# Optimization experiments

Hardware: AMD Instinct MI355X
Metric: run time of the kernel (lower is better)

Reference implementation:

```python
import jax, jax.numpy as jnp
import numpy as np
import math

N_PATCH = 32768
DIM = 512
L_TOK = 64
W_SIZE = 64
STRIDE = 32


def setup_inputs() -> dict:
    key = jax.random.key(0)
    ks = jax.random.split(key, 12)
    d = DIM
    inp = {
        'feats': jax.random.normal(ks[0], (N_PATCH, d), dtype=jnp.float32),
        'coords': jax.random.uniform(ks[1], (N_PATCH, 2), dtype=jnp.float32),
        'mask': jnp.zeros((N_PATCH,), dtype=bool),
        'z': jax.random.normal(ks[2], (L_TOK, d), dtype=jnp.float32),
        'Wq': jax.random.normal(ks[3], (d, d), dtype=jnp.float32) / math.sqrt(d),
        'Wk': jax.random.normal(ks[4], (d, d), dtype=jnp.float32) / math.sqrt(d),
        'Wv': jax.random.normal(ks[5], (d, d), dtype=jnp.float32) / math.sqrt(d),
        'w1': jax.random.normal(ks[6], (d, 2), dtype=jnp.float32) / math.sqrt(2.0),
        'b1': jnp.zeros((d,), dtype=jnp.float32),
        'w2': jax.random.normal(ks[7], (d, d), dtype=jnp.float32) / math.sqrt(d),
        'b2': jnp.zeros((d,), dtype=jnp.float32),
        'Wo': jax.random.normal(ks[8], (d, d), dtype=jnp.float32) / math.sqrt(d),
        'bo': jnp.zeros((d,), dtype=jnp.float32),
    }
    return inp


def _lstcwa(feats, coords, z, Wq, Wk, Wv, w1, b1, w2, b2, Wo, bo):
    # mask is all-False -> feats kept as-is; N divisible by L -> equal segments
    N, D = feats.shape
    L = z.shape[0]
    n = N // L                       # patches per segment
    nwin = -(-n // STRIDE)           # windows per segment (ceil)

    # window offsets within a segment, [nwin, w]; last window truncated via mask
    off = jnp.arange(nwin)[:, None] * STRIDE + jnp.arange(W_SIZE)[None, :]
    valid = off < n                  # [nwin, w]
    idx = jnp.arange(L)[:, None, None] * n + jnp.minimum(off, n - 1)[None]  # [L,nwin,w]

    q = z @ Wq.T                     # [L, D]
    kf = feats @ Wk.T                # [N, D]
    vf = feats @ Wv.T

    k_win = kf[idx]                  # [L, nwin, w, D]
    v_win = vf[idx]
    c_win = coords[idx]              # [L, nwin, w, 2]

    vf32 = valid.astype(feats.dtype)                      # [nwin, w]
    cnt = vf32.sum(-1)                                    # [nwin]
    c_mean = jnp.einsum('lnwc,nw->lnc', c_win, vf32) / cnt[None, :, None]
    delta = (c_win - c_mean[:, :, None, :]) * vf32[None, :, :, None]

    pos = jax.nn.relu(delta @ w1.T + b1) @ w2.T + b2      # [L, nwin, w, D]
    k_win = k_win + pos

    logits = jnp.einsum('ld,lnwd->lnw', q, k_win) / math.sqrt(D)
    logits = jnp.where(valid[None], logits, -1e9)
    attn = jax.nn.softmax(logits, axis=-1)                # [L, nwin, w]

    z_win = jnp.einsum('lnw,lnwd->lnd', attn, v_win)      # [L, nwin, D]
    # return_alpha=False path: z_l_acc / max(1, len(attn_acc)=0) -> SUM over windows
    Z = z_win.sum(1)                                      # [L, D]
    return Z @ Wo.T + bo


def reference(feats, coords, mask, z, Wq, Wk, Wv, w1, b1, w2, b2, Wo, bo):
    # mask is all-False by construction (static shapes under jit)
    return _lstcwa(feats, coords, z, Wq, Wk, Wv, w1, b1, w2, b2, Wo, bo)
```

## Files before the change

### kernel.cpp

```cpp
#include <hip/hip_runtime.h>
#include <math.h>

#define DIMV 512
#define LTOK 64
#define SEG  512
#define NWIN 16
#define WSZ  64
#define INV_SQRT_D 0.044194173824159216f

__device__ __forceinline__ float wave_sum(float v) {
#pragma unroll
  for (int m = 1; m < 64; m <<= 1) v += __shfl_xor(v, m, 64);
  return v;
}
__device__ __forceinline__ float wave_max(float v) {
#pragma unroll
  for (int m = 1; m < 64; m <<= 1) v = fmaxf(v, __shfl_xor(v, m, 64));
  return v;
}

__global__ __launch_bounds__(256, 4) void k_q(const float* __restrict__ z,
    const float* __restrict__ Wq, float* __restrict__ q)
{
  int l = blockIdx.x >> 4, c = blockIdx.x & 15;
  int wave = threadIdx.x >> 6, lane = threadIdx.x & 63;
  int e0 = lane << 3;
  const float* zp = z + l * DIMV + e0;
  float x0[8];
  *(float4*)&x0[0] = *(const float4*)zp;
  *(float4*)&x0[4] = *(const float4*)(zp + 4);
  int d0 = c * 32 + wave * 8;
  float rf[8][8];
#pragma unroll
  for (int k = 0; k < 8; ++k) {
    const float* rp = Wq + (size_t)(d0 + k) * DIMV + e0;
    *(float4*)&rf[k][0] = *(const float4*)rp;
    *(float4*)&rf[k][4] = *(const float4*)(rp + 4);
  }
#pragma unroll
  for (int k = 0; k < 8; ++k) {
    float p = 0.f;
#pragma unroll
    for (int j = 0; j < 8; ++j) p = fmaf(rf[k][j], x0[j], p);
    p = wave_sum(p);
    if (lane == k) q[l * DIMV + d0 + k] = p;
  }
}

__global__ __launch_bounds__(256) void k_qproj(const float* __restrict__ q,
    const float* __restrict__ Wk, const float* __restrict__ w2,
    const float* __restrict__ b2, float* __restrict__ qk,
    float* __restrict__ qw2, float* __restrict__ qb2)
{
  int l = blockIdx.x >> 3, ec = blockIdx.x & 7;
  int wave = threadIdx.x >> 6, lane = threadIdx.x & 63;
  int t = threadIdx.x;
  __shared__ float qs[DIMV];
  __shared__ float pk[4][64], pw[4][64];
  qs[t] = q[l * DIMV + t];
  qs[t + 256] = q[l * DIMV + t + 256];
  __syncthreads();
  int e = ec * 64 + lane;
  int d0 = wave * 128;
  float ak = 0.f, aw = 0.f;
#pragma unroll 8
  for (int dd = 0; dd < 128; ++dd) {
    int d = d0 + dd;
    float qd = qs[d];
    ak = fmaf(qd, Wk[(size_t)d * DIMV + e], ak);
    aw = fmaf(qd, w2[(size_t)d * DIMV + e], aw);
  }
  pk[wave][lane] = ak;
  pw[wave][lane] = aw;
  __syncthreads();
  if (wave == 0) {
    qk[l * DIMV + e] = pk[0][lane] + pk[1][lane] + pk[2][lane] + pk[3][lane];
  } else if (wave == 1) {
    qw2[l * DIMV + e] = pw[0][lane] + pw[1][lane] + pw[2][lane] + pw[3][lane];
  } else if (wave == 2 && ec == 0) {
    int e0 = lane << 3;
    float pb = 0.f;
#pragma unroll
    for (int j = 0; j < 8; ++j) pb = fmaf(qs[e0 + j], b2[e0 + j], pb);
    pb = wave_sum(pb);
    if (lane == 0) qb2[l] = pb;
  }
}

__global__ __launch_bounds__(512, 2) void k_attn(
    const float* __restrict__ feats, const float* __restrict__ coords,
    const float* __restrict__ qk,  const float* __restrict__ qw2,
    const float* __restrict__ qb2, const float* __restrict__ w1,
    const float* __restrict__ b1,  float* __restrict__ upart)
{
  int bid = blockIdx.x;
  int swz = (bid & 7) * 128 + (bid >> 3);
  int l = swz >> 4, n = swz & 15;
  int wave = threadIdx.x >> 6, lane = threadIdx.x & 63;
  int e0 = lane << 3;

  __shared__ float dxs[WSZ], dys[WSZ], lg[WSZ];
  __shared__ float upacc[8][DIMV];

  int base = n * 32;
  int nvalid = SEG - base; if (nvalid > WSZ) nvalid = WSZ;
  const float* fwin = feats + ((size_t)l * SEG + base) * DIMV;

  float rf[8][8];
#pragma unroll
  for (int k = 0; k < 8; ++k) {
    int r = wave * 8 + k;
    if (r < nvalid) {
      const float* rp = fwin + (size_t)r * DIMV + e0;
      *(float4*)&rf[k][0] = *(const float4*)rp;
      *(float4*)&rf[k][4] = *(const float4*)(rp + 4);
    } else {
#pragma unroll
      for (int j = 0; j < 8; ++j) rf[k][j] = 0.f;
    }
  }

  float qk8[8], qw8[8], w1a[8], w1b[8], b18[8];
  {
    const float* p = qk + l * DIMV + e0;
    *(float4*)&qk8[0] = *(const float4*)p;
    *(float4*)&qk8[4] = *(const float4*)(p + 4);
    p = qw2 + l * DIMV + e0;
    *(float4*)&qw8[0] = *(const float4*)p;
    *(float4*)&qw8[4] = *(const float4*)(p + 4);
    float w1v[16];
#pragma unroll
    for (int i = 0; i < 4; ++i) *(float4*)&w1v[i * 4] = *(const float4*)(w1 + e0 * 2 + i * 4);
#pragma unroll
    for (int j = 0; j < 8; ++j) { w1a[j] = w1v[2 * j]; w1b[j] = w1v[2 * j + 1]; }
    p = b1 + e0;
    *(float4*)&b18[0] = *(const float4*)p;
    *(float4*)&b18[4] = *(const float4*)(p + 4);
  }
  float qb2l = qb2[l];

  if (wave == 0) {
    bool v = lane < nvalid;
    float cx = 0.f, cy = 0.f;
    if (v) {
      const float* cp = coords + ((size_t)(l * SEG + base + lane)) * 2;
      cx = cp[0]; cy = cp[1];
    }
    float inv = 1.0f / (float)nvalid;
    float mx = wave_sum(cx) * inv;
    float my = wave_sum(cy) * inv;
    dxs[lane] = v ? cx - mx : 0.f;
    dys[lane] = v ? cy - my : 0.f;
  }

#pragma unroll
  for (int k = 0; k < 8; ++k)
#pragma unroll
    for (int j = 0; j < 8; ++j)
      asm volatile("" : "+v"(rf[k][j]));
  __syncthreads();

#pragma unroll
  for (int k = 0; k < 8; ++k) {
    int r = wave * 8 + k;
    float dx = dxs[r], dy = dys[r];
    float p = 0.f;
#pragma unroll
    for (int j = 0; j < 8; ++j) {
      float h = fmaf(dx, w1a[j], fmaf(dy, w1b[j], b18[j]));
      p = fmaf(fmaxf(h, 0.f), qw8[j], p);
      p = fmaf(qk8[j], rf[k][j], p);
    }
    p = wave_sum(p);
    if (lane == k) lg[r] = (r < nvalid) ? (p + qb2l) * INV_SQRT_D : -1e9f;
  }
  __syncthreads();

  float my_attn;
  {
    float v = lg[lane];
    float m = wave_max(v);
    float ex = __expf(v - m);
    float s = wave_sum(ex);
    my_attn = ex / s;
  }

  float u8[8];
#pragma unroll
  for (int j = 0; j < 8; ++j) u8[j] = 0.f;
#pragma unroll
  for (int k = 0; k < 8; ++k) {
    float a = __shfl(my_attn, wave * 8 + k, 64);
#pragma unroll
    for (int j = 0; j < 8; ++j) u8[j] = fmaf(a, rf[k][j], u8[j]);
  }
  *(float4*)&upacc[wave][e0]     = *(float4*)&u8[0];
  *(float4*)&upacc[wave][e0 + 4] = *(float4*)&u8[4];
  __syncthreads();
  int t = threadIdx.x;
  float acc = 0.f;
#pragma unroll
  for (int wv = 0; wv < 8; ++wv) acc += upacc[wv][t];
  upart[((size_t)(l * NWIN) + n) * DIMV + t] = acc;
}

__global__ __launch_bounds__(512) void k_ured(const float* __restrict__ upart,
    float* __restrict__ U)
{
  int l = blockIdx.x, t = threadIdx.x;
  float a = 0.f;
#pragma unroll
  for (int n = 0; n < NWIN; ++n) a += upart[((size_t)(l * NWIN) + n) * DIMV + t];
  U[l * DIMV + t] = a;
}

__global__ __launch_bounds__(256, 4) void k_uv(const float* __restrict__ U,
    const float* __restrict__ Wv, float* __restrict__ tbuf)
{
  int l = blockIdx.x >> 4, c = blockIdx.x & 15;
  int wave = threadIdx.x >> 6, lane = threadIdx.x & 63;
  int e0 = lane << 3;
  const float* up = U + l * DIMV + e0;
  float x0[8];
  *(float4*)&x0[0] = *(const float4*)up;
  *(float4*)&x0[4] = *(const float4*)(up + 4);
  int f0 = c * 32 + wave * 8;
  float rf[8][8];
#pragma unroll
  for (int k = 0; k < 8; ++k) {
    const float* rp = Wv + (size_t)(f0 + k) * DIMV + e0;
    *(float4*)&rf[k][0] = *(const float4*)rp;
    *(float4*)&rf[k][4] = *(const float4*)(rp + 4);
  }
#pragma unroll
  for (int k = 0; k < 8; ++k) {
    float p = 0.f;
#pragma unroll
    for (int j = 0; j < 8; ++j) p = fmaf(rf[k][j], x0[j], p);
    p = wave_sum(p);
    if (lane == k) tbuf[l * DIMV + f0 + k] = p;
  }
}

__global__ __launch_bounds__(256, 4) void k_out(const float* __restrict__ tbuf,
    const float* __restrict__ Wo, const float* __restrict__ bo,
    float* __restrict__ out)
{
  int l = blockIdx.x >> 4, c = blockIdx.x & 15;
  int wave = threadIdx.x >> 6, lane = threadIdx.x & 63;
  int e0 = lane << 3;
  const float* tp = tbuf + l * DIMV + e0;
  float x0[8];
  *(float4*)&x0[0] = *(const float4*)tp;
  *(float4*)&x0[4] = *(const float4*)(tp + 4);
  int d0 = c * 32 + wave * 8;
  float rf[8][8];
#pragma unroll
  for (int k = 0; k < 8; ++k) {
    const float* rp = Wo + (size_t)(d0 + k) * DIMV + e0;
    *(float4*)&rf[k][0] = *(const float4*)rp;
    *(float4*)&rf[k][4] = *(const float4*)(rp + 4);
  }
#pragma unroll
  for (int k = 0; k < 8; ++k) {
    float p = 0.f;
#pragma unroll
    for (int j = 0; j < 8; ++j) p = fmaf(rf[k][j], x0[j], p);
    p = wave_sum(p);
    if (lane == k) out[l * DIMV + d0 + k] = p + bo[d0 + k];
  }
}

extern "C" void kernel_launch(void* const* d_in, const int* in_sizes, int n_in,
                              void* d_out, int out_size, void* d_ws, size_t ws_size,
                              hipStream_t stream) {
  (void)in_sizes; (void)n_in; (void)out_size; (void)ws_size;
  const float* feats  = (const float*)d_in[0];
  const float* coords = (const float*)d_in[1];
  const float* z   = (const float*)d_in[3];
  const float* Wq  = (const float*)d_in[4];
  const float* Wk  = (const float*)d_in[5];
  const float* Wv  = (const float*)d_in[6];
  const float* w1  = (const float*)d_in[7];
  const float* b1  = (const float*)d_in[8];
  const float* w2  = (const float*)d_in[9];
  const float* b2  = (const float*)d_in[10];
  const float* Wo  = (const float*)d_in[11];
  const float* bo  = (const float*)d_in[12];
  float* out = (float*)d_out;

  float* q     = (float*)d_ws;
  float* qk    = q     + LTOK * DIMV;
  float* qw2   = qk    + LTOK * DIMV;
  float* qb2   = qw2   + LTOK * DIMV;
  float* U     = qb2   + LTOK;
  float* tbuf  = U     + LTOK * DIMV;
  float* upart = tbuf  + LTOK * DIMV;

  hipLaunchKernelGGL(k_q,     dim3(LTOK * 16), dim3(256), 0, stream, z, Wq, q);
  hipLaunchKernelGGL(k_qproj, dim3(LTOK * 8),  dim3(256), 0, stream,
                     q, Wk, w2, b2, qk, qw2, qb2);
  hipLaunchKernelGGL(k_attn,  dim3(LTOK * NWIN), dim3(512), 0, stream,
                     feats, coords, qk, qw2, qb2, w1, b1, upart);
  hipLaunchKernelGGL(k_ured,  dim3(LTOK),      dim3(512), 0, stream, upart, U);
  hipLaunchKernelGGL(k_uv,    dim3(LTOK * 16), dim3(256), 0, stream, U, Wv, tbuf);
  hipLaunchKernelGGL(k_out,   dim3(LTOK * 16), dim3(256), 0, stream, tbuf, Wo, bo, out);
}
```

Before: 56.22 us.

## Share feature rows across overlapping windows and split positional logits into own kernel

The attention kernel now processes 96-row chunks covering two overlapping windows per block. Each feature row is loaded once and its q·k dot product is reused by both windows, which removes the 2x redundant reads of feats caused by stride-32 windows of width 64. The positional-MLP logit term moves into a separate k_pos kernel that uses per-window coordinate means computed in k_q. The upart reduction is folded into k_uv, dropping the k_ured launch. The trade-off is an extra kernel with a serial 512-length loop per lane and a lower occupancy bound of 1 block per CU for k_attn, which now holds 96 registers of feature data.

```diff
diff --git a/kernel.cpp b/kernel.cpp
--- a/kernel.cpp
+++ b/kernel.cpp
@@ -6,6 +6,7 @@
 #define SEG  512
 #define NWIN 16
 #define WSZ  64
+#define NB   8
 #define INV_SQRT_D 0.044194173824159216f
 
 __device__ __forceinline__ float wave_sum(float v) {
@@ -20,7 +21,8 @@
 }
 
 __global__ __launch_bounds__(256, 4) void k_q(const float* __restrict__ z,
-    const float* __restrict__ Wq, float* __restrict__ q)
+    const float* __restrict__ Wq, const float* __restrict__ coords,
+    float* __restrict__ q, float* __restrict__ cmean)
 {
   int l = blockIdx.x >> 4, c = blockIdx.x & 15;
   int wave = threadIdx.x >> 6, lane = threadIdx.x & 63;
@@ -44,6 +46,23 @@
     for (int j = 0; j < 8; ++j) p = fmaf(rf[k][j], x0[j], p);
     p = wave_sum(p);
     if (lane == k) q[l * DIMV + d0 + k] = p;
+  }
+  if (wave == 0) {
+    int n = c;
+    int nvalid = (n == 15) ? 32 : 64;
+    bool v = lane < nvalid;
+    float cx = 0.f, cy = 0.f;
+    if (v) {
+      const float* cp = coords + ((size_t)(l * SEG + n * 32 + lane)) * 2;
+      cx = cp[0]; cy = cp[1];
+    }
+    float inv = 1.0f / (float)nvalid;
+    float mx = wave_sum(cx) * inv;
+    float my = wave_sum(cy) * inv;
+    if (lane == 0) {
+      cmean[(l * NWIN + n) * 2]     = mx;
+      cmean[(l * NWIN + n) * 2 + 1] = my;
+    }
   }
 }
 
@@ -87,31 +106,55 @@
   }
 }
 
-__global__ __launch_bounds__(512, 2) void k_attn(
-    const float* __restrict__ feats, const float* __restrict__ coords,
-    const float* __restrict__ qk,  const float* __restrict__ qw2,
-    const float* __restrict__ qb2, const float* __restrict__ w1,
-    const float* __restrict__ b1,  float* __restrict__ upart)
+__global__ __launch_bounds__(256) void k_pos(const float* __restrict__ coords,
+    const float* __restrict__ cmean, const float* __restrict__ qw2,
+    const float* __restrict__ w1, const float* __restrict__ b1,
+    float* __restrict__ pos)
+{
+  int widx = blockIdx.x * 4 + (threadIdx.x >> 6);
+  int lane = threadIdx.x & 63;
+  int l = widx >> 4, n = widx & 15;
+  int off = n * 32 + lane;
+  int row = (off < SEG) ? off : SEG - 1;
+  const float* cp = coords + ((size_t)(l * SEG + row)) * 2;
+  float cx = cp[0], cy = cp[1];
+  float mx = cmean[(l * NWIN + n) * 2], my = cmean[(l * NWIN + n) * 2 + 1];
+  float dx = cx - mx, dy = cy - my;
+  const float* qwp = qw2 + l * DIMV;
+  float acc = 0.f;
+#pragma unroll 8
+  for (int d = 0; d < DIMV; ++d) {
+    float2 wv = *(const float2*)(w1 + 2 * d);
+    float h = fmaf(dx, wv.x, fmaf(dy, wv.y, b1[d]));
+    acc = fmaf(fmaxf(h, 0.f), qwp[d], acc);
+  }
+  pos[(size_t)widx * WSZ + lane] = acc;
+}
+
+__global__ __launch_bounds__(512, 1) void k_attn(
+    const float* __restrict__ feats, const float* __restrict__ qk,
+    const float* __restrict__ qb2, const float* __restrict__ pos,
+    float* __restrict__ upart)
 {
   int bid = blockIdx.x;
-  int swz = (bid & 7) * 128 + (bid >> 3);
-  int l = swz >> 4, n = swz & 15;
-  int wave = threadIdx.x >> 6, lane = threadIdx.x & 63;
-  int e0 = lane << 3;
-
-  __shared__ float dxs[WSZ], dys[WSZ], lg[WSZ];
+  int swz = (bid & 7) * 64 + (bid >> 3);
+  int l = swz >> 3, c = swz & 7;
+  int wave = threadIdx.x >> 6, lane = threadIdx.x & 63;
+  int e0 = lane << 3, t = threadIdx.x;
+  int rows = SEG - 64 * c; if (rows > 96) rows = 96;
+
+  __shared__ float dts[96];
+  __shared__ float attA[WSZ], attB[WSZ];
   __shared__ float upacc[8][DIMV];
 
-  int base = n * 32;
-  int nvalid = SEG - base; if (nvalid > WSZ) nvalid = WSZ;
-  const float* fwin = feats + ((size_t)l * SEG + base) * DIMV;
-
-  float rf[8][8];
-#pragma unroll
-  for (int k = 0; k < 8; ++k) {
-    int r = wave * 8 + k;
-    if (r < nvalid) {
-      const float* rp = fwin + (size_t)r * DIMV + e0;
+  const float* fbase = feats + ((size_t)(l * SEG + c * 64)) * DIMV;
+
+  float rf[12][8];
+#pragma unroll
+  for (int k = 0; k < 12; ++k) {
+    int r = wave * 12 + k;
+    if (r < rows) {
+      const float* rp = fbase + (size_t)r * DIMV + e0;
       *(float4*)&rf[k][0] = *(const float4*)rp;
       *(float4*)&rf[k][4] = *(const float4*)(rp + 4);
     } else {
@@ -119,111 +162,89 @@
       for (int j = 0; j < 8; ++j) rf[k][j] = 0.f;
     }
   }
-
-  float qk8[8], qw8[8], w1a[8], w1b[8], b18[8];
+  float qk8[8];
   {
     const float* p = qk + l * DIMV + e0;
     *(float4*)&qk8[0] = *(const float4*)p;
     *(float4*)&qk8[4] = *(const float4*)(p + 4);
-    p = qw2 + l * DIMV + e0;
-    *(float4*)&qw8[0] = *(const float4*)p;
-    *(float4*)&qw8[4] = *(const float4*)(p + 4);
-    float w1v[16];
-#pragma unroll
-    for (int i = 0; i < 4; ++i) *(float4*)&w1v[i * 4] = *(const float4*)(w1 + e0 * 2 + i * 4);
-#pragma unroll
-    for (int j = 0; j < 8; ++j) { w1a[j] = w1v[2 * j]; w1b[j] = w1v[2 * j + 1]; }
-    p = b1 + e0;
-    *(float4*)&b18[0] = *(const float4*)p;
-    *(float4*)&b18[4] = *(const float4*)(p + 4);
   }
   float qb2l = qb2[l];
 
-  if (wave == 0) {
-    bool v = lane < nvalid;
-    float cx = 0.f, cy = 0.f;
-    if (v) {
-      const float* cp = coords + ((size_t)(l * SEG + base + lane)) * 2;
-      cx = cp[0]; cy = cp[1];
-    }
-    float inv = 1.0f / (float)nvalid;
-    float mx = wave_sum(cx) * inv;
-    float my = wave_sum(cy) * inv;
-    dxs[lane] = v ? cx - mx : 0.f;
-    dys[lane] = v ? cy - my : 0.f;
-  }
-
-#pragma unroll
-  for (int k = 0; k < 8; ++k)
+#pragma unroll
+  for (int k = 0; k < 12; ++k)
 #pragma unroll
     for (int j = 0; j < 8; ++j)
       asm volatile("" : "+v"(rf[k][j]));
-  __syncthreads();
-
-#pragma unroll
-  for (int k = 0; k < 8; ++k) {
-    int r = wave * 8 + k;
-    float dx = dxs[r], dy = dys[r];
+
+#pragma unroll
+  for (int k = 0; k < 12; ++k) {
+    int r = wave * 12 + k;
     float p = 0.f;
 #pragma unroll
-    for (int j = 0; j < 8; ++j) {
-      float h = fmaf(dx, w1a[j], fmaf(dy, w1b[j], b18[j]));
-      p = fmaf(fmaxf(h, 0.f), qw8[j], p);
-      p = fmaf(qk8[j], rf[k][j], p);
+    for (int j = 0; j < 8; ++j) p = fmaf(qk8[j], rf[k][j], p);
+    p = wave_sum(p);
+    if (lane == k && r < rows) dts[r] = p;
+  }
+  __syncthreads();
+
+  const float* posA = pos + ((size_t)(l * NWIN) + 2 * c) * WSZ;
+  const float* posB = posA + WSZ;
+  if (wave == 0) {
+    float lg = (dts[lane] + posA[lane] + qb2l) * INV_SQRT_D;
+    float m = wave_max(lg);
+    float ex = __expf(lg - m);
+    float s = wave_sum(ex);
+    attA[lane] = ex / s;
+  } else if (wave == 1) {
+    int r = 32 + lane;
+    float lg = (r < rows) ? (dts[r] + posB[lane] + qb2l) * INV_SQRT_D : -1e9f;
+    float m = wave_max(lg);
+    float ex = __expf(lg - m);
+    float s = wave_sum(ex);
+    attB[lane] = ex / s;
+  }
+  __syncthreads();
+
+  float u8[8];
+#pragma unroll
+  for (int j = 0; j < 8; ++j) u8[j] = 0.f;
+#pragma unroll
+  for (int k = 0; k < 12; ++k) {
+    int r = wave * 12 + k;
+    if (r < rows) {
+      float g = 0.f;
+      if (r < 64)  g += attA[r];
+      if (r >= 32) g += attB[r - 32];
+#pragma unroll
+      for (int j = 0; j < 8; ++j) u8[j] = fmaf(g, rf[k][j], u8[j]);
     }
-    p = wave_sum(p);
-    if (lane == k) lg[r] = (r < nvalid) ? (p + qb2l) * INV_SQRT_D : -1e9f;
-  }
-  __syncthreads();
-
-  float my_attn;
-  {
-    float v = lg[lane];
-    float m = wave_max(v);
-    float ex = __expf(v - m);
-    float s = wave_sum(ex);
-    my_attn = ex / s;
-  }
-
-  float u8[8];
-#pragma unroll
-  for (int j = 0; j < 8; ++j) u8[j] = 0.f;
-#pragma unroll
-  for (int k = 0; k < 8; ++k) {
-    float a = __shfl(my_attn, wave * 8 + k, 64);
-#pragma unroll
-    for (int j = 0; j < 8; ++j) u8[j] = fmaf(a, rf[k][j], u8[j]);
   }
   *(float4*)&upacc[wave][e0]     = *(float4*)&u8[0];
   *(float4*)&upacc[wave][e0 + 4] = *(float4*)&u8[4];
   __syncthreads();
-  int t = threadIdx.x;
-  float acc = 0.f;
-#pragma unroll
-  for (int wv = 0; wv < 8; ++wv) acc += upacc[wv][t];
-  upart[((size_t)(l * NWIN) + n) * DIMV + t] = acc;
-}
-
-__global__ __launch_bounds__(512) void k_ured(const float* __restrict__ upart,
-    float* __restrict__ U)
-{
-  int l = blockIdx.x, t = threadIdx.x;
   float a = 0.f;
 #pragma unroll
-  for (int n = 0; n < NWIN; ++n) a += upart[((size_t)(l * NWIN) + n) * DIMV + t];
-  U[l * DIMV + t] = a;
-}
-
-__global__ __launch_bounds__(256, 4) void k_uv(const float* __restrict__ U,
+  for (int wv = 0; wv < 8; ++wv) a += upacc[wv][t];
+  upart[((size_t)(l * NB) + c) * DIMV + t] = a;
+}
+
+__global__ __launch_bounds__(256, 4) void k_uv(const float* __restrict__ upart,
     const float* __restrict__ Wv, float* __restrict__ tbuf)
 {
   int l = blockIdx.x >> 4, c = blockIdx.x & 15;
   int wave = threadIdx.x >> 6, lane = threadIdx.x & 63;
   int e0 = lane << 3;
-  const float* up = U + l * DIMV + e0;
-  float x0[8];
-  *(float4*)&x0[0] = *(const float4*)up;
-  *(float4*)&x0[4] = *(const float4*)(up + 4);
+  float u8[8];
+#pragma unroll
+  for (int j = 0; j < 8; ++j) u8[j] = 0.f;
+#pragma unroll
+  for (int cc = 0; cc < NB; ++cc) {
+    const float* up = upart + ((size_t)(l * NB) + cc) * DIMV + e0;
+    float4 a = *(const float4*)up;
+    float4 b = *(const float4*)(up + 4);
+    u8[0] += a.x; u8[1] += a.y; u8[2] += a.z; u8[3] += a.w;
+    u8[4] += b.x; u8[5] += b.y; u8[6] += b.z; u8[7] += b.w;
+  }
   int f0 = c * 32 + wave * 8;
   float rf[8][8];
 #pragma unroll
@@ -236,7 +257,7 @@
   for (int k = 0; k < 8; ++k) {
     float p = 0.f;
 #pragma unroll
-    for (int j = 0; j < 8; ++j) p = fmaf(rf[k][j], x0[j], p);
+    for (int j = 0; j < 8; ++j) p = fmaf(rf[k][j], u8[j], p);
     p = wave_sum(p);
     if (lane == k) tbuf[l * DIMV + f0 + k] = p;
   }
@@ -293,16 +314,21 @@
   float* qk    = q     + LTOK * DIMV;
   float* qw2   = qk    + LTOK * DIMV;
   float* qb2   = qw2   + LTOK * DIMV;
-  float* U     = qb2   + LTOK;
-  float* tbuf  = U     + LTOK * DIMV;
+  float* cmean = qb2   + LTOK;
+  float* pos   = cmean + LTOK * NWIN * 2;
+  float* tbuf  = pos   + LTOK * NWIN * WSZ;
   float* upart = tbuf  + LTOK * DIMV;
 
-  hipLaunchKernelGGL(k_q,     dim3(LTOK * 16), dim3(256), 0, stream, z, Wq, q);
-  hipLaunchKernelGGL(k_qproj, dim3(LTOK * 8),  dim3(256), 0, stream,
+  hipLaunchKernelGGL(k_q,     dim3(LTOK * NWIN), dim3(256), 0, stream,
+                     z, Wq, coords, q, cmean);
+  hipLaunchKernelGGL(k_qproj, dim3(LTOK * 8),    dim3(256), 0, stream,
                      q, Wk, w2, b2, qk, qw2, qb2);
-  hipLaunchKernelGGL(k_attn,  dim3(LTOK * NWIN), dim3(512), 0, stream,
-                     feats, coords, qk, qw2, qb2, w1, b1, upart);
-  hipLaunchKernelGGL(k_ured,  dim3(LTOK),      dim3(512), 0, stream, upart, U);
-  hipLaunchKernelGGL(k_uv,    dim3(LTOK * 16), dim3(256), 0, stream, U, Wv, tbuf);
-  hipLaunchKernelGGL(k_out,   dim3(LTOK * 16), dim3(256), 0, stream, tbuf, Wo, bo, out);
-}
+  hipLaunchKernelGGL(k_pos,   dim3(LTOK * NWIN / 4), dim3(256), 0, stream,
+                     coords, cmean, qw2, w1, b1, pos);
+  hipLaunchKernelGGL(k_attn,  dim3(LTOK * NB),   dim3(512), 0, stream,
+                     feats, qk, qb2, pos, upart);
+  hipLaunchKernelGGL(k_uv,    dim3(LTOK * NWIN), dim3(256), 0, stream,
+                     upart, Wv, tbuf);
+  hipLaunchKernelGGL(k_out,   dim3(LTOK * NWIN), dim3(256), 0, stream,
+                     tbuf, Wo, bo, out);
+}
```

Result: slower. 78.19 us (+39.1%).
